# Kernel optimization log

Hardware: AMD Instinct MI355X
Metric: run time of the kernel (lower is better)

Reference implementation:

```python
import jax, jax.numpy as jnp
import numpy as np
import math

B, S, E, H, DK = 2, 2048, 1024, 16, 64  # batch, seq, embed, heads, d_k (= n_wires)

def setup_inputs() -> dict:
    key = jax.random.key(0)
    k1, k2, k3, k4, k5 = jax.random.split(key, 5)
    scale = 0.02
    return {
        "x": jax.random.normal(k1, (B, S, E), dtype=jnp.float32),
        "Wk": jax.random.normal(k2, (E, E), dtype=jnp.float32) * scale,
        "Wv": jax.random.normal(k3, (E, E), dtype=jnp.float32) * scale,
        "Wq": jax.random.normal(k4, (H, DK, E), dtype=jnp.float32) * scale,
        "theta": jax.random.normal(k5, (DK,), dtype=jnp.float32) * scale,
    }

def reference(x, Wk, Wv, Wq, theta):
    batch, seq, embed = x.shape
    n_heads, d_k = Wq.shape[0], Wq.shape[1]
    # K, V projections (nn.Linear, no bias): x @ W.T
    k = (x @ Wk.T).reshape(batch, seq, n_heads, d_k).transpose(0, 2, 1, 3)  # [B,H,S,dk]
    v = (x @ Wv.T).reshape(batch, seq, n_heads, d_k).transpose(0, 2, 1, 3)  # [B,H,S,dk]
    # Quantum query path: per-head linear proj -> RX(proj_i) then RX(theta_i) on wire i from |0>,
    # MeasureAll(PauliZ) on independent wires gives <Z_i> = cos(proj_i + theta_i) exactly.
    proj = jnp.einsum('bse,hde->bhsd', x, Wq)          # [B,H,S,dk]
    q = jnp.cos(proj + theta)                           # [B,H,S,dk]
    scores = jnp.einsum('bhsd,bhtd->bhst', q, k) / math.sqrt(d_k)  # [B,H,S,S]
    attn = jax.nn.softmax(scores, axis=-1)
    out = jnp.einsum('bhst,bhtd->bhsd', attn, v)        # [B,H,S,dk]
    return out.transpose(0, 2, 1, 3).reshape(batch, seq, embed)
```

## Files before the change

kernel.cpp:

```cpp
#include <hip/hip_runtime.h>
#include <hip/hip_bf16.h>

constexpr int B  = 2;
constexpr int S  = 2048;
constexpr int E  = 1024;
constexpr int H  = 16;
constexpr int DK = 64;
constexpr int M  = B * S;
constexpr int N3 = 3 * E;
constexpr long RSZ = (long)B * H * S * DK;

#define QSCALE 0.18033688011112042f

using bf16x8 = __attribute__((ext_vector_type(8))) __bf16;
using bf16x4 = __attribute__((ext_vector_type(4))) __bf16;
using f32x4  = __attribute__((ext_vector_type(4))) float;

__device__ __forceinline__ void async16(__bf16* lds, const __bf16* g) {
    __builtin_amdgcn_global_load_lds(
        (const __attribute__((address_space(1))) void*)g,
        (__attribute__((address_space(3))) void*)lds, 16, 0, 0);
}

__global__ __launch_bounds__(256)
void cvt_kernel(const float* __restrict__ x, const float* __restrict__ Wk,
                const float* __restrict__ Wv, const float* __restrict__ Wq,
                __bf16* __restrict__ xb, __bf16* __restrict__ wall) {
    const long e = ((long)blockIdx.x * 256 + threadIdx.x) * 4;
    const float* src;
    __bf16* dst;
    if (e < (long)M * E) { src = x + e; dst = xb + e; }
    else {
        const long e2 = e - (long)M * E;
        const int which = (int)(e2 >> 20);
        const long off  = e2 & ((1L << 20) - 1);
        src = (which == 0 ? Wk : which == 1 ? Wv : Wq) + off;
        dst = wall + e2;
    }
    float4 f = *reinterpret_cast<const float4*>(src);
    bf16x4 o;
    o[0] = (__bf16)f.x; o[1] = (__bf16)f.y; o[2] = (__bf16)f.z; o[3] = (__bf16)f.w;
    *reinterpret_cast<bf16x4*>(dst) = o;
}

__global__ __launch_bounds__(256, 3)
void qkv_gemm(const __bf16* __restrict__ xb, const __bf16* __restrict__ wall,
              const float* __restrict__ theta, __bf16* __restrict__ kvq) {
    __shared__ __align__(1024) __bf16 smem[6 * 128 * 32];
    __bf16* tile = smem;

    const int t    = threadIdx.x;
    const int lane = t & 63;
    const int w    = t >> 6;
    const int quad = lane >> 4;
    const int l16  = lane & 15;
    const int wm   = w >> 1, wn = w & 1;
    const int mbase = blockIdx.y * 128;
    const int nbase = blockIdx.x * 128;

    f32x4 acc[4][4];
    #pragma unroll
    for (int i = 0; i < 4; i++)
        #pragma unroll
        for (int j = 0; j < 4; j++)
            acc[i][j] = f32x4{0.f, 0.f, 0.f, 0.f};

    const int srow = lane >> 2;
    const int srcc = (lane & 3) ^ ((lane >> 3) & 3);
    const __bf16* ga = xb   + (long)(mbase + srow) * E + srcc * 8;
    const __bf16* gb = wall + (long)(nbase + srow) * E + srcc * 8;

    const int csw = (l16 >> 1) & 3;

    #pragma unroll
    for (int pt = 0; pt < 2; pt++) {
        #pragma unroll
        for (int c = 0; c < 2; c++) {
            async16(smem + pt * 4096 +         (c * 64 + w * 16) * 32,
                    ga + (long)(c * 64 + w * 16) * E + pt * 32);
            async16(smem + pt * 4096 + 12288 + (c * 64 + w * 16) * 32,
                    gb + (long)(c * 64 + w * 16) * E + pt * 32);
        }
    }

    int cur = 0;
    constexpr int ITERS = E / 32;
    for (int it = 0; it < ITERS; it++) {
        if (it < ITERS - 1) asm volatile("s_waitcnt vmcnt(4)" ::: "memory");
        else                asm volatile("s_waitcnt vmcnt(0)" ::: "memory");
        asm volatile("s_barrier" ::: "memory");

        if (it + 2 < ITERS) {
            const int pb  = (cur == 0) ? 2 : cur - 1;
            const int kk2 = (it + 2) * 32;
            #pragma unroll
            for (int c = 0; c < 2; c++) {
                async16(smem + pb * 4096 +         (c * 64 + w * 16) * 32,
                        ga + (long)(c * 64 + w * 16) * E + kk2);
                async16(smem + pb * 4096 + 12288 + (c * 64 + w * 16) * 32,
                        gb + (long)(c * 64 + w * 16) * E + kk2);
            }
        }

        const __bf16* Asb = smem + cur * 4096;
        const __bf16* Bsb = smem + cur * 4096 + 12288;
        bf16x8 a[4], b[4];
        #pragma unroll
        for (int i = 0; i < 4; i++)
            a[i] = *reinterpret_cast<const bf16x8*>(
                &Asb[(wm * 64 + i * 16 + l16) * 32 + (quad ^ csw) * 8]);
        #pragma unroll
        for (int j = 0; j < 4; j++)
            b[j] = *reinterpret_cast<const bf16x8*>(
                &Bsb[(wn * 64 + j * 16 + l16) * 32 + (quad ^ csw) * 8]);
        #pragma unroll
        for (int i = 0; i < 4; i++)
            #pragma unroll
            for (int j = 0; j < 4; j++)
                acc[i][j] = __builtin_amdgcn_mfma_f32_16x16x32_bf16(a[i], b[j], acc[i][j], 0, 0, 0);

        cur = (cur == 2) ? 0 : cur + 1;
    }

    const int region = nbase >> 10;
    const int bb = mbase >> 11;
    if (region == 1) {
        __syncthreads();
        #pragma unroll
        for (int i = 0; i < 4; i++) {
            const int cchunk = wm * 8 + i * 2 + (quad >> 1);
            #pragma unroll
            for (int j = 0; j < 4; j++) {
                const int cirb = wn * 64 + j * 16 + l16;
                const int cs = cchunk ^ l16;
                bf16x4 pk;
                #pragma unroll
                for (int r = 0; r < 4; r++) pk[r] = (__bf16)acc[i][j][r];
                *reinterpret_cast<bf16x4*>(&tile[cirb * 128 + cs * 8 + (quad & 1) * 4]) = pk;
            }
        }
        __syncthreads();
        const int h0 = (nbase & 1023) >> 6;
        __bf16* vt = kvq + RSZ;
        #pragma unroll
        for (int p = 0; p < 8; p++) {
            const int dcol = p * 16 + (t >> 4);
            const int lc = t & 15;
            const int cs2 = lc ^ (dcol & 15);
            bf16x8 vv = *reinterpret_cast<const bf16x8*>(&tile[dcol * 128 + cs2 * 8]);
            const int hh = h0 + (dcol >> 6), d = dcol & 63;
            *reinterpret_cast<bf16x8*>(
                &vt[((long)(bb * H + hh) * DK + d) * S + (mbase & 2047) + lc * 8]) = vv;
        }
    } else {
        __bf16* dst = kvq + (region == 2 ? 2 * RSZ : 0);
        float th[4];
        if (region == 2) {
            #pragma unroll
            for (int j = 0; j < 4; j++) th[j] = theta[j * 16 + l16];
        }
        #pragma unroll
        for (int i = 0; i < 4; i++) {
            const int row0 = mbase + wm * 64 + i * 16 + quad * 4;
            #pragma unroll
            for (int j = 0; j < 4; j++) {
                const int cir = (nbase & 1023) + wn * 64 + j * 16 + l16;
                const int h = cir >> 6, d = cir & 63;
                #pragma unroll
                for (int r = 0; r < 4; r++) {
                    const int s = (row0 + r) & 2047;
                    float v = acc[i][j][r];
                    if (region == 2) v = cosf(v + th[j]) * QSCALE;
                    dst[((long)(bb * H + h) * S + s) * DK + d] = (__bf16)v;
                }
            }
        }
    }
}

__global__ __launch_bounds__(256, 2)
void attn_kernel(const __bf16* __restrict__ q_ws, const __bf16* __restrict__ k_ws,
                 const __bf16* __restrict__ v_ws, float* __restrict__ out) {
    __shared__ __align__(1024) __bf16 Ks[3][64 * 64];
    __shared__ __align__(1024) __bf16 Vs[3][64 * 64];
    __shared__ __align__(16)   __bf16 Pl[4][32 * 72];
    __shared__ __align__(16)   float  ls_lds[4][32];

    const int lane = threadIdx.x & 63;
    const int w    = threadIdx.x >> 6;
    const int quad = lane >> 4;
    const int l16  = lane & 15;

    const int id    = blockIdx.x;
    const int bh    = (id & 7) + 8 * ((id >> 3) & 3);
    const int qbase = (id >> 5) * 128 + w * 32;

    const __bf16* qp = q_ws + (long)bh * S * DK;
    const __bf16* kp = k_ws + (long)bh * S * DK;
    const __bf16* vp = v_ws + (long)bh * DK * S;

    const int sr  = lane >> 3;
    const int scs = (lane & 7) ^ sr;

    bf16x8 bq[2][2];
    #pragma unroll
    for (int nt = 0; nt < 2; nt++)
        #pragma unroll
        for (int ks = 0; ks < 2; ks++)
            bq[nt][ks] = *reinterpret_cast<const bf16x8*>(
                qp + (long)(qbase + nt * 16 + l16) * DK + ks * 32 + quad * 8);

    f32x4 o[2][4];
    #pragma unroll
    for (int i = 0; i < 2; i++)
        #pragma unroll
        for (int j = 0; j < 4; j++) o[i][j] = f32x4{0.f, 0.f, 0.f, 0.f};
    float lsum[2] = {0.f, 0.f};

    #pragma unroll
    for (int pt = 0; pt < 2; pt++) {
        #pragma unroll
        for (int i = 0; i < 2; i++) {
            const int row = w * 16 + i * 8;
            async16(&Ks[pt][row * 64], kp + (long)(pt * 64 + row + sr) * DK + scs * 8);
            async16(&Vs[pt][row * 64], vp + (long)(row + sr) * S + pt * 64 + scs * 8);
        }
    }

    int cur = 0;
    constexpr int ITERS = S / 64;
    for (int it = 0; it < ITERS; it++) {
        if (it < ITERS - 1) asm volatile("s_waitcnt vmcnt(4)" ::: "memory");
        else                asm volatile("s_waitcnt vmcnt(0)" ::: "memory");
        asm volatile("s_barrier" ::: "memory");

        if (it + 2 < ITERS) {
            const int kt2 = (it + 2) * 64;
            const int pb  = (cur == 0) ? 2 : cur - 1;
            #pragma unroll
            for (int i = 0; i < 2; i++) {
                const int row = w * 16 + i * 8;
                async16(&Ks[pb][row * 64], kp + (long)(kt2 + row + sr) * DK + scs * 8);
                async16(&Vs[pb][row * 64], vp + (long)(row + sr) * S + kt2 + scs * 8);
            }
        }

        f32x4 sacc[4][2];
        #pragma unroll
        for (int i = 0; i < 4; i++)
            #pragma unroll
            for (int j = 0; j < 2; j++) sacc[i][j] = f32x4{0.f, 0.f, 0.f, 0.f};
        #pragma unroll
        for (int ks = 0; ks < 2; ks++) {
            bf16x8 ak[4];
            #pragma unroll
            for (int mt = 0; mt < 4; mt++)
                ak[mt] = *reinterpret_cast<const bf16x8*>(
                    &Ks[cur][(mt * 16 + l16) * 64 + ((ks * 4 + quad) ^ (l16 & 7)) * 8]);
            #pragma unroll
            for (int mt = 0; mt < 4; mt++)
                #pragma unroll
                for (int nt = 0; nt < 2; nt++)
                    sacc[mt][nt] = __builtin_amdgcn_mfma_f32_16x16x32_bf16(
                        ak[mt], bq[nt][ks], sacc[mt][nt], 0, 0, 0);
        }

        #pragma unroll
        for (int mt = 0; mt < 4; mt++)
            #pragma unroll
            for (int nt = 0; nt < 2; nt++) {
                float p0 = __builtin_amdgcn_exp2f(sacc[mt][nt][0]);
                float p1 = __builtin_amdgcn_exp2f(sacc[mt][nt][1]);
                float p2 = __builtin_amdgcn_exp2f(sacc[mt][nt][2]);
                float p3 = __builtin_amdgcn_exp2f(sacc[mt][nt][3]);
                lsum[nt] += (p0 + p1) + (p2 + p3);
                bf16x4 pk;
                pk[0] = (__bf16)p0; pk[1] = (__bf16)p1;
                pk[2] = (__bf16)p2; pk[3] = (__bf16)p3;
                *reinterpret_cast<bf16x4*>(
                    &Pl[w][(nt * 16 + l16) * 72 + mt * 16 + quad * 4]) = pk;
            }

        #pragma unroll
        for (int kh = 0; kh < 2; kh++) {
            bf16x8 bv[4];
            #pragma unroll
            for (int nt = 0; nt < 4; nt++)
                bv[nt] = *reinterpret_cast<const bf16x8*>(
                    &Vs[cur][(nt * 16 + l16) * 64 + ((kh * 4 + quad) ^ (l16 & 7)) * 8]);
            #pragma unroll
            for (int mt = 0; mt < 2; mt++) {
                bf16x8 ap = *reinterpret_cast<const bf16x8*>(
                    &Pl[w][(mt * 16 + l16) * 72 + kh * 32 + quad * 8]);
                #pragma unroll
                for (int nt = 0; nt < 4; nt++)
                    o[mt][nt] = __builtin_amdgcn_mfma_f32_16x16x32_bf16(
                        ap, bv[nt], o[mt][nt], 0, 0, 0);
            }
        }

        cur = (cur == 2) ? 0 : cur + 1;
    }

    #pragma unroll
    for (int nt = 0; nt < 2; nt++) {
        float v = lsum[nt];
        v += __shfl_xor(v, 16);
        v += __shfl_xor(v, 32);
        ls_lds[w][nt * 16 + l16] = v;
    }

    const int b = bh >> 4, h = bh & 15;
    #pragma unroll
    for (int mt = 0; mt < 2; mt++) {
        f32x4 lv = *reinterpret_cast<const f32x4*>(&ls_lds[w][mt * 16 + quad * 4]);
        #pragma unroll
        for (int r = 0; r < 4; r++) {
            const float inv = 1.0f / lv[r];
            const int srow = qbase + mt * 16 + quad * 4 + r;
            #pragma unroll
            for (int nt = 0; nt < 4; nt++)
                out[(long)(b * S + srow) * E + h * DK + nt * 16 + l16] = o[mt][nt][r] * inv;
        }
    }
}

__device__ inline bf16x8 cvt_frag(const float* __restrict__ p) {
    float4 f0 = *reinterpret_cast<const float4*>(p);
    float4 f1 = *reinterpret_cast<const float4*>(p + 4);
    bf16x8 r;
    r[0] = (__bf16)f0.x; r[1] = (__bf16)f0.y; r[2] = (__bf16)f0.z; r[3] = (__bf16)f0.w;
    r[4] = (__bf16)f1.x; r[5] = (__bf16)f1.y; r[6] = (__bf16)f1.z; r[7] = (__bf16)f1.w;
    return r;
}
template <int MODE>
__global__ __launch_bounds__(256, 2)
void proj_kernel(const float* __restrict__ x, const float* __restrict__ W,
                 const float* __restrict__ theta, __bf16* __restrict__ out) {
    const int lane = threadIdx.x & 63;
    const int w    = threadIdx.x >> 6;
    const int quad = lane >> 4;
    const int l16  = lane & 15;
    const int mbase = blockIdx.y * 128 + w * 32;
    const int nbase = blockIdx.x * 128;
    f32x4 acc[2][8];
    #pragma unroll
    for (int i = 0; i < 2; i++)
        #pragma unroll
        for (int j = 0; j < 8; j++) acc[i][j] = f32x4{0.f, 0.f, 0.f, 0.f};
    float th[4];
    if (MODE == 2) {
        #pragma unroll
        for (int j = 0; j < 4; j++) th[j] = theta[j * 16 + l16];
    }
    for (int kk = 0; kk < E; kk += 32) {
        bf16x8 a[2], b[8];
        #pragma unroll
        for (int mt = 0; mt < 2; mt++)
            a[mt] = cvt_frag(x + (long)(mbase + mt * 16 + l16) * E + kk + quad * 8);
        #pragma unroll
        for (int nt = 0; nt < 8; nt++)
            b[nt] = cvt_frag(W + (long)(nbase + nt * 16 + l16) * E + kk + quad * 8);
        #pragma unroll
        for (int mt = 0; mt < 2; mt++)
            #pragma unroll
            for (int nt = 0; nt < 8; nt++)
                acc[mt][nt] = __builtin_amdgcn_mfma_f32_16x16x32_bf16(a[mt], b[nt], acc[mt][nt], 0, 0, 0);
    }
    #pragma unroll
    for (int mt = 0; mt < 2; mt++) {
        const int row0 = mbase + mt * 16 + quad * 4;
        #pragma unroll
        for (int nt = 0; nt < 8; nt++) {
            const int col = nbase + nt * 16 + l16;
            const int h = col >> 6, d = col & 63;
            #pragma unroll
            for (int r = 0; r < 4; r++) {
                const int row = row0 + r;
                const int bb = row >> 11, s = row & 2047;
                float v = acc[mt][nt][r];
                if (MODE == 2) v = cosf(v + th[nt & 3]) * QSCALE;
                long idx;
                if (MODE == 1) idx = ((long)(bb * H + h) * DK + d) * S + s;
                else           idx = ((long)(bb * H + h) * S + s) * DK + d;
                out[idx] = (__bf16)v;
            }
        }
    }
}

extern "C" void kernel_launch(void* const* d_in, const int* in_sizes, int n_in,
                              void* d_out, int out_size, void* d_ws, size_t ws_size,
                              hipStream_t stream) {
    const float* x     = (const float*)d_in[0];
    const float* Wk    = (const float*)d_in[1];
    const float* Wv    = (const float*)d_in[2];
    const float* Wq    = (const float*)d_in[3];
    const float* theta = (const float*)d_in[4];
    float* out = (float*)d_out;

    __bf16* kvq  = (__bf16*)d_ws;
    __bf16* xb   = kvq + 3 * RSZ;
    __bf16* wall = xb + (long)M * E;
    __bf16* k_ws = kvq;
    __bf16* v_t  = kvq + RSZ;
    __bf16* q_ws = kvq + 2 * RSZ;

    const size_t need = (3 * RSZ + (long)M * E + (long)N3 * E) * 2;
    dim3 blk(256);
    if (ws_size >= need) {
        cvt_kernel<<<dim3(7168), blk, 0, stream>>>(x, Wk, Wv, Wq, xb, wall);
        qkv_gemm<<<dim3(N3 / 128, M / 128), blk, 0, stream>>>(xb, wall, theta, kvq);
    } else {
        dim3 gp(E / 128, M / 128);
        proj_kernel<0><<<gp, blk, 0, stream>>>(x, Wk, nullptr, k_ws);
        proj_kernel<1><<<gp, blk, 0, stream>>>(x, Wv, nullptr, v_t);
        proj_kernel<2><<<gp, blk, 0, stream>>>(x, Wq, theta, q_ws);
    }

    attn_kernel<<<dim3(512), blk, 0, stream>>>(q_ws, k_ws, v_t, out);
}
```

Before: 173.1 us.

## Stage bf16 operands in output buffer and drop LDS transpose for V

```diff
diff --git a/kernel.cpp b/kernel.cpp
--- a/kernel.cpp
+++ b/kernel.cpp
@@ -47,7 +47,6 @@
 void qkv_gemm(const __bf16* __restrict__ xb, const __bf16* __restrict__ wall,
               const float* __restrict__ theta, __bf16* __restrict__ kvq) {
     __shared__ __align__(1024) __bf16 smem[6 * 128 * 32];
-    __bf16* tile = smem;
 
     const int t    = threadIdx.x;
     const int lane = t & 63;
@@ -124,48 +123,28 @@
 
     const int region = nbase >> 10;
     const int bb = mbase >> 11;
-    if (region == 1) {
-        __syncthreads();
-        #pragma unroll
-        for (int i = 0; i < 4; i++) {
-            const int cchunk = wm * 8 + i * 2 + (quad >> 1);
-            #pragma unroll
-            for (int j = 0; j < 4; j++) {
-                const int cirb = wn * 64 + j * 16 + l16;
-                const int cs = cchunk ^ l16;
+    __bf16* vt = kvq + RSZ;
+    __bf16* dst = kvq + (region == 2 ? 2 * RSZ : 0);
+    float th[4];
+    if (region == 2) {
+        #pragma unroll
+        for (int j = 0; j < 4; j++) th[j] = theta[j * 16 + l16];
+    }
+    #pragma unroll
+    for (int i = 0; i < 4; i++) {
+        const int row0 = mbase + wm * 64 + i * 16 + quad * 4;
+        #pragma unroll
+        for (int j = 0; j < 4; j++) {
+            const int cir = (nbase & 1023) + wn * 64 + j * 16 + l16;
+            const int h = cir >> 6, d = cir & 63;
+            if (region == 1) {
                 bf16x4 pk;
                 #pragma unroll
                 for (int r = 0; r < 4; r++) pk[r] = (__bf16)acc[i][j][r];
-                *reinterpret_cast<bf16x4*>(&tile[cirb * 128 + cs * 8 + (quad & 1) * 4]) = pk;
-            }
-        }
-        __syncthreads();
-        const int h0 = (nbase & 1023) >> 6;
-        __bf16* vt = kvq + RSZ;
-        #pragma unroll
-        for (int p = 0; p < 8; p++) {
-            const int dcol = p * 16 + (t >> 4);
-            const int lc = t & 15;
-            const int cs2 = lc ^ (dcol & 15);
-            bf16x8 vv = *reinterpret_cast<const bf16x8*>(&tile[dcol * 128 + cs2 * 8]);
-            const int hh = h0 + (dcol >> 6), d = dcol & 63;
-            *reinterpret_cast<bf16x8*>(
-                &vt[((long)(bb * H + hh) * DK + d) * S + (mbase & 2047) + lc * 8]) = vv;
-        }
-    } else {
-        __bf16* dst = kvq + (region == 2 ? 2 * RSZ : 0);
-        float th[4];
-        if (region == 2) {
-            #pragma unroll
-            for (int j = 0; j < 4; j++) th[j] = theta[j * 16 + l16];
-        }
-        #pragma unroll
-        for (int i = 0; i < 4; i++) {
-            const int row0 = mbase + wm * 64 + i * 16 + quad * 4;
-            #pragma unroll
-            for (int j = 0; j < 4; j++) {
-                const int cir = (nbase & 1023) + wn * 64 + j * 16 + l16;
-                const int h = cir >> 6, d = cir & 63;
+                const int s0 = row0 & 2047;
+                *reinterpret_cast<bf16x4*>(
+                    &vt[((long)(bb * H + h) * DK + d) * S + s0]) = pk;
+            } else {
                 #pragma unroll
                 for (int r = 0; r < 4; r++) {
                     const int s = (row0 + r) & 2047;
@@ -325,70 +304,6 @@
     }
 }
 
-__device__ inline bf16x8 cvt_frag(const float* __restrict__ p) {
-    float4 f0 = *reinterpret_cast<const float4*>(p);
-    float4 f1 = *reinterpret_cast<const float4*>(p + 4);
-    bf16x8 r;
-    r[0] = (__bf16)f0.x; r[1] = (__bf16)f0.y; r[2] = (__bf16)f0.z; r[3] = (__bf16)f0.w;
-    r[4] = (__bf16)f1.x; r[5] = (__bf16)f1.y; r[6] = (__bf16)f1.z; r[7] = (__bf16)f1.w;
-    return r;
-}
-template <int MODE>
-__global__ __launch_bounds__(256, 2)
-void proj_kernel(const float* __restrict__ x, const float* __restrict__ W,
-                 const float* __restrict__ theta, __bf16* __restrict__ out) {
-    const int lane = threadIdx.x & 63;
-    const int w    = threadIdx.x >> 6;
-    const int quad = lane >> 4;
-    const int l16  = lane & 15;
-    const int mbase = blockIdx.y * 128 + w * 32;
-    const int nbase = blockIdx.x * 128;
-    f32x4 acc[2][8];
-    #pragma unroll
-    for (int i = 0; i < 2; i++)
-        #pragma unroll
-        for (int j = 0; j < 8; j++) acc[i][j] = f32x4{0.f, 0.f, 0.f, 0.f};
-    float th[4];
-    if (MODE == 2) {
-        #pragma unroll
-        for (int j = 0; j < 4; j++) th[j] = theta[j * 16 + l16];
-    }
-    for (int kk = 0; kk < E; kk += 32) {
-        bf16x8 a[2], b[8];
-        #pragma unroll
-        for (int mt = 0; mt < 2; mt++)
-            a[mt] = cvt_frag(x + (long)(mbase + mt * 16 + l16) * E + kk + quad * 8);
-        #pragma unroll
-        for (int nt = 0; nt < 8; nt++)
-            b[nt] = cvt_frag(W + (long)(nbase + nt * 16 + l16) * E + kk + quad * 8);
-        #pragma unroll
-        for (int mt = 0; mt < 2; mt++)
-            #pragma unroll
-            for (int nt = 0; nt < 8; nt++)
-                acc[mt][nt] = __builtin_amdgcn_mfma_f32_16x16x32_bf16(a[mt], b[nt], acc[mt][nt], 0, 0, 0);
-    }
-    #pragma unroll
-    for (int mt = 0; mt < 2; mt++) {
-        const int row0 = mbase + mt * 16 + quad * 4;
-        #pragma unroll
-        for (int nt = 0; nt < 8; nt++) {
-            const int col = nbase + nt * 16 + l16;
-            const int h = col >> 6, d = col & 63;
-            #pragma unroll
-            for (int r = 0; r < 4; r++) {
-                const int row = row0 + r;
-                const int bb = row >> 11, s = row & 2047;
-                float v = acc[mt][nt][r];
-                if (MODE == 2) v = cosf(v + th[nt & 3]) * QSCALE;
-                long idx;
-                if (MODE == 1) idx = ((long)(bb * H + h) * DK + d) * S + s;
-                else           idx = ((long)(bb * H + h) * S + s) * DK + d;
-                out[idx] = (__bf16)v;
-            }
-        }
-    }
-}
-
 extern "C" void kernel_launch(void* const* d_in, const int* in_sizes, int n_in,
                               void* d_out, int out_size, void* d_ws, size_t ws_size,
                               hipStream_t stream) {
@@ -400,23 +315,14 @@
     float* out = (float*)d_out;
 
     __bf16* kvq  = (__bf16*)d_ws;
-    __bf16* xb   = kvq + 3 * RSZ;
-    __bf16* wall = xb + (long)M * E;
     __bf16* k_ws = kvq;
     __bf16* v_t  = kvq + RSZ;
     __bf16* q_ws = kvq + 2 * RSZ;
-
-    const size_t need = (3 * RSZ + (long)M * E + (long)N3 * E) * 2;
+    __bf16* xb   = (__bf16*)d_out;
+    __bf16* wall = xb + (long)M * E;
+
     dim3 blk(256);
-    if (ws_size >= need) {
-        cvt_kernel<<<dim3(7168), blk, 0, stream>>>(x, Wk, Wv, Wq, xb, wall);
-        qkv_gemm<<<dim3(N3 / 128, M / 128), blk, 0, stream>>>(xb, wall, theta, kvq);
-    } else {
-        dim3 gp(E / 128, M / 128);
-        proj_kernel<0><<<gp, blk, 0, stream>>>(x, Wk, nullptr, k_ws);
-        proj_kernel<1><<<gp, blk, 0, stream>>>(x, Wv, nullptr, v_t);
-        proj_kernel<2><<<gp, blk, 0, stream>>>(x, Wq, theta, q_ws);
-    }
-
+    cvt_kernel<<<dim3(7168), blk, 0, stream>>>(x, Wk, Wv, Wq, xb, wall);
+    qkv_gemm<<<dim3(N3 / 128, M / 128), blk, 0, stream>>>(xb, wall, theta, kvq);
     attn_kernel<<<dim3(512), blk, 0, stream>>>(q_ws, k_ws, v_t, out);
 }
```

After: 173.6 us. About the same (+0.3%).
